# Optimization experiments

Hardware: AMD Instinct MI355X
Metric: run time of the kernel (lower is better)

Reference implementation:

```python
import jax, jax.numpy as jnp
import numpy as np

D_STATE = 16
DT_RANK = 4


def selective_scan(u, delta, A, Bc, Cc, D):
    """Mamba selective scan.
    u, delta: [S, L, d]; A: [d, N]; Bc, Cc: [S, L, N]; D: [d].
    Returns y: [S, L, d].
    """
    # discretize: deltaA [S,L,d,N], deltaB*u [S,L,d,N]
    dA = jnp.exp(delta[..., None] * A)
    dBu = (delta * u)[..., None] * Bc[:, :, None, :]

    def step(h, inp):
        dA_t, dBu_t, C_t = inp  # [S,d,N], [S,d,N], [S,N]
        h = dA_t * h + dBu_t
        y = jnp.einsum('sdn,sn->sd', h, C_t)
        return h, y

    S, L, d = u.shape
    N = A.shape[1]
    h0 = jnp.zeros((S, d, N), u.dtype)
    _, ys = jax.lax.scan(
        step, h0,
        (dA.transpose(1, 0, 2, 3), dBu.transpose(1, 0, 2, 3), Cc.transpose(1, 0, 2)))
    y = ys.transpose(1, 0, 2)  # [S, L, d]
    return y + u * D


def ssm_branch(u, A_log, D, x_proj_w, dt_proj_w, dt_proj_b):
    """u: [S, L, d] sequence of tokens; applies input-dependent SSM."""
    N = A_log.shape[1]
    proj = jnp.einsum('sld,pd->slp', u, x_proj_w)  # [S,L,dt_rank+2N]
    dt_raw = proj[..., :DT_RANK]
    Bc = proj[..., DT_RANK:DT_RANK + N]
    Cc = proj[..., DT_RANK + N:]
    delta = jax.nn.softplus(jnp.einsum('slr,dr->sld', dt_raw, dt_proj_w) + dt_proj_b)
    A = -jnp.exp(A_log)  # [d, N]
    return selective_scan(u, delta, A, Bc, Cc, D)


def setup_inputs() -> dict:
    key = jax.random.key(0)
    ks = jax.random.split(key, 6)
    B, C, H, W = 4, 64, 128, 128
    x = jax.random.normal(ks[0], (B, C, H, W), jnp.float32)
    A_log = jnp.log(jax.random.uniform(ks[1], (C, D_STATE), jnp.float32, 0.5, 4.0))
    D = jax.random.normal(ks[2], (C,), jnp.float32)
    x_proj_w = jax.random.normal(ks[3], (DT_RANK + 2 * D_STATE, C), jnp.float32) * (C ** -0.5)
    dt_proj_w = jax.random.normal(ks[4], (C, DT_RANK), jnp.float32) * (DT_RANK ** -0.5)
    dt_proj_b = jax.random.normal(ks[5], (C,), jnp.float32) * 0.1
    return {"x": x, "A_log": A_log, "D": D, "x_proj_w": x_proj_w,
            "dt_proj_w": dt_proj_w, "dt_proj_b": dt_proj_b}


def reference(x, A_log, D, x_proj_w, dt_proj_w, dt_proj_b):
    B, C, H, W = x.shape
    # horizontal scan: B*H row-sequences of length W
    u_h = x.transpose(0, 2, 3, 1).reshape(B * H, W, C)
    y_h = ssm_branch(u_h, A_log, D, x_proj_w, dt_proj_w, dt_proj_b)
    y_h = y_h.reshape(B, H, W, C).transpose(0, 3, 1, 2)
    # vertical scan: B*W column-sequences of length H
    u_v = x.transpose(0, 3, 2, 1).reshape(B * W, H, C)
    y_v = ssm_branch(u_v, A_log, D, x_proj_w, dt_proj_w, dt_proj_b)
    y_v = y_v.reshape(B, W, H, C).transpose(0, 3, 2, 1)
    return y_h + y_v
```

## Files before the change

kernel.cpp:

```cpp
#include <hip/hip_runtime.h>

#define BB 4
#define CC 64
#define HH 128
#define WW 128
#define NN 16
#define HW (HH*WW)

#if __has_builtin(__builtin_amdgcn_exp2f)
#define EXP2F(x) __builtin_amdgcn_exp2f(x)
#else
#define EXP2F(x) exp2f(x)
#endif

__device__ __forceinline__ float softplus_f(float x) {
    float e = __expf(-fabsf(x));
    return fmaxf(x, 0.0f) + __logf(1.0f + e);
}

__device__ __forceinline__ float2 f2mul(float2 a, float2 b) {
    return make_float2(a.x * b.x, a.y * b.y);
}
__device__ __forceinline__ float2 f2fma(float2 a, float2 b, float2 c) {
    return make_float2(fmaf(a.x, b.x, c.x), fmaf(a.y, b.y, c.y));
}

__global__ __launch_bounds__(256) void k_scan(
    const float* __restrict__ x, const float* __restrict__ xpw,
    const float* __restrict__ A_log, const float* __restrict__ Dv,
    const float* __restrict__ dtw, const float* __restrict__ dtb,
    float* __restrict__ out, float* __restrict__ yv)
{
    __shared__ float xt[128 * 64];
    __shared__ float bcs[128 * 32];
    __shared__ float dtr[128 * 4];
    __shared__ float dlt[8 * 64];

    const int t = threadIdx.x;
    const int half = blockIdx.x >> 9;
    const int r9 = blockIdx.x & 511;
    const int b = r9 >> 7;
    const int L = r9 & 127;

    if (half == 0) {
#pragma unroll
        for (int k = 0; k < 8; ++k) {
            int i = k * 256 + t;
            int c = i >> 5, jq = i & 31;
            float4 v = *(const float4*)&x[((size_t)(b * CC + c) * HH + L) * WW + jq * 4];
            int j0 = jq * 4;
            xt[(j0 + 0) * 64 + ((c + j0 + 0) & 63)] = v.x;
            xt[(j0 + 1) * 64 + ((c + j0 + 1) & 63)] = v.y;
            xt[(j0 + 2) * 64 + ((c + j0 + 2) & 63)] = v.z;
            xt[(j0 + 3) * 64 + ((c + j0 + 3) & 63)] = v.w;
        }
    } else {
#pragma unroll
        for (int p = 0; p < 32; ++p) {
            int c = t & 63, j = p * 4 + (t >> 6);
            xt[j * 64 + ((c + j) & 63)] =
                x[((size_t)(b * CC + c) * HH + j) * WW + L];
        }
    }
    __syncthreads();

    {
        const int wv = t >> 6, lane = t & 63;
        const int pg2 = __builtin_amdgcn_readfirstlane(wv & 1);
        const int pix = (wv >> 1) * 64 + lane;
        const int p0 = pg2 * 18;
        const int sw = pix & 7;
        float acc[18];
#pragma unroll
        for (int j = 0; j < 18; ++j) acc[j] = 0.f;
        for (int c4 = 0; c4 < 16; ++c4) {
            float xv0 = xt[pix * 64 + ((c4 * 4 + 0 + pix) & 63)];
            float xv1 = xt[pix * 64 + ((c4 * 4 + 1 + pix) & 63)];
            float xv2 = xt[pix * 64 + ((c4 * 4 + 2 + pix) & 63)];
            float xv3 = xt[pix * 64 + ((c4 * 4 + 3 + pix) & 63)];
#pragma unroll
            for (int j = 0; j < 18; ++j) {
                float4 wq = *(const float4*)&xpw[(p0 + j) * CC + c4 * 4];
                acc[j] = fmaf(wq.x, xv0, fmaf(wq.y, xv1,
                         fmaf(wq.z, xv2, fmaf(wq.w, xv3, acc[j]))));
            }
        }
        float* bp = &bcs[pix * 32];
        if (pg2 == 0) {
            *(float4*)&dtr[pix * 4] = make_float4(acc[0], acc[1], acc[2], acc[3]);
            *(float4*)&bp[((0 ^ sw) << 2)] = make_float4(acc[4], acc[5], acc[6], acc[7]);
            *(float4*)&bp[((1 ^ sw) << 2)] = make_float4(acc[8], acc[9], acc[10], acc[11]);
            *(float4*)&bp[((2 ^ sw) << 2)] = make_float4(acc[12], acc[13], acc[14], acc[15]);
            bp[((3 ^ sw) << 2) + 0] = acc[16];
            bp[((3 ^ sw) << 2) + 1] = acc[17];
        } else {
            bp[((3 ^ sw) << 2) + 2] = acc[0];
            bp[((3 ^ sw) << 2) + 3] = acc[1];
            *(float4*)&bp[((4 ^ sw) << 2)] = make_float4(acc[2], acc[3], acc[4], acc[5]);
            *(float4*)&bp[((5 ^ sw) << 2)] = make_float4(acc[6], acc[7], acc[8], acc[9]);
            *(float4*)&bp[((6 ^ sw) << 2)] = make_float4(acc[10], acc[11], acc[12], acc[13]);
            *(float4*)&bp[((7 ^ sw) << 2)] = make_float4(acc[14], acc[15], acc[16], acc[17]);
        }
    }

    const int d = t >> 2, ng = t & 3, n0 = ng * 4;
    const float L2E = 1.44269504088896340736f;
    float A0 = -__expf(A_log[d * NN + n0 + 0]) * L2E;
    float A1 = -__expf(A_log[d * NN + n0 + 1]) * L2E;
    float A2 = -__expf(A_log[d * NN + n0 + 2]) * L2E;
    float A3 = -__expf(A_log[d * NN + n0 + 3]) * L2E;
    const float Dd = Dv[d];
    float2 h01 = make_float2(0.f, 0.f), h23 = make_float2(0.f, 0.f);
    const int dd = t & 63, jb = t >> 6;
    const float4 wt4 = *(const float4*)&dtw[dd * 4];
    const float bdd = dtb[dd];
    float* drow = (half == 0 ? out : yv) + ((size_t)(b * CC + d) * 128 + L) * 128;

    for (int ch = 0; ch < 16; ++ch) {
        __syncthreads();
#pragma unroll
        for (int k = 0; k < 2; ++k) {
            int jl = jb * 2 + k;
            float4 dr = *(const float4*)&dtr[(ch * 8 + jl) * 4];
            float draw = fmaf(dr.x, wt4.x, fmaf(dr.y, wt4.y,
                         fmaf(dr.z, wt4.z, fmaf(dr.w, wt4.w, bdd))));
            dlt[jl * 64 + dd] = softplus_f(draw);
        }
        __syncthreads();
        float y0 = 0.f, y1 = 0.f;
#pragma unroll
        for (int jl = 0; jl < 8; ++jl) {
            const int j = ch * 8 + jl;
            float delta = dlt[jl * 64 + d];
            float u = xt[j * 64 + ((d + j) & 63)];
            const int s = j & 7;
            float4 Bv = *(const float4*)&bcs[j * 32 + ((ng ^ s) << 2)];
            float4 Cv = *(const float4*)&bcs[j * 32 + (((4 + ng) ^ s) << 2)];
            float du = delta * u;
            float2 e01 = make_float2(EXP2F(delta * A0), EXP2F(delta * A1));
            float2 e23 = make_float2(EXP2F(delta * A2), EXP2F(delta * A3));
            float2 du2 = make_float2(du, du);
            h01 = f2fma(e01, h01, f2mul(du2, make_float2(Bv.x, Bv.y)));
            h23 = f2fma(e23, h23, f2mul(du2, make_float2(Bv.z, Bv.w)));
            float2 yt = f2fma(h23, make_float2(Cv.z, Cv.w),
                              f2mul(h01, make_float2(Cv.x, Cv.y)));
            float y = yt.x + yt.y;
            y += __shfl_xor(y, 1);
            y += __shfl_xor(y, 2);
            y = fmaf(u, Dd, y);
            if (ng == (jl >> 1)) { if (jl & 1) y1 = y; else y0 = y; }
        }
        *(float2*)&drow[ch * 8 + ng * 2] = make_float2(y0, y1);
    }
}

__global__ __launch_bounds__(256) void k_add(const float* __restrict__ yv,
                                             float* __restrict__ out)
{
    __shared__ float td[32 * 33];
    int t = threadIdx.x;
    int bc_ = blockIdx.x >> 4;
    int tb = blockIdx.x & 15;
    int w0 = (tb & 3) * 32;
    int h0 = (tb >> 2) * 32;
    const float* src = yv + (size_t)bc_ * HW;
    float* dst = out + (size_t)bc_ * HW;
    int r = t >> 3, q = t & 7;
    float4 v = *(const float4*)&src[(w0 + r) * HH + h0 + q * 4];
    td[r * 33 + q * 4 + 0] = v.x;
    td[r * 33 + q * 4 + 1] = v.y;
    td[r * 33 + q * 4 + 2] = v.z;
    td[r * 33 + q * 4 + 3] = v.w;
    __syncthreads();
    float* op = &dst[(h0 + r) * WW + w0 + q * 4];
    float4 o = *(float4*)op;
    o.x += td[(q * 4 + 0) * 33 + r];
    o.y += td[(q * 4 + 1) * 33 + r];
    o.z += td[(q * 4 + 2) * 33 + r];
    o.w += td[(q * 4 + 3) * 33 + r];
    *(float4*)op = o;
}

extern "C" void kernel_launch(void* const* d_in, const int* in_sizes, int n_in,
                              void* d_out, int out_size, void* d_ws, size_t ws_size,
                              hipStream_t stream) {
    const float* x     = (const float*)d_in[0];
    const float* A_log = (const float*)d_in[1];
    const float* Dv    = (const float*)d_in[2];
    const float* xpw   = (const float*)d_in[3];
    const float* dtw   = (const float*)d_in[4];
    const float* dtb   = (const float*)d_in[5];
    float* out = (float*)d_out;
    float* yv  = (float*)d_ws;

    k_scan<<<1024, 256, 0, stream>>>(x, xpw, A_log, Dv, dtw, dtb, out, yv);
    k_add <<<BB * CC * 16, 256, 0, stream>>>(yv, out);
}
```

Baseline: 149.9 us.

## Fuse vertical-scan accumulation into scan via atomics, drop transpose-add kernel

Splits the single scan launch into two sequential launches (horizontal, then vertical). The vertical pass accumulates its results directly into the output with atomicAdd instead of writing a workspace buffer. This removes the separate transpose-and-add kernel and its extra read/write of a full-size intermediate. In exchange, the vertical pass issues strided scalar atomics (stride 128 floats), which coalesce poorly, and the two halves can no longer overlap within one grid.

```diff
diff --git a/kernel.cpp b/kernel.cpp
--- a/kernel.cpp
+++ b/kernel.cpp
@@ -29,7 +29,7 @@
     const float* __restrict__ x, const float* __restrict__ xpw,
     const float* __restrict__ A_log, const float* __restrict__ Dv,
     const float* __restrict__ dtw, const float* __restrict__ dtb,
-    float* __restrict__ out, float* __restrict__ yv)
+    float* __restrict__ out, int half)
 {
     __shared__ float xt[128 * 64];
     __shared__ float bcs[128 * 32];
@@ -37,10 +37,8 @@
     __shared__ float dlt[8 * 64];
 
     const int t = threadIdx.x;
-    const int half = blockIdx.x >> 9;
-    const int r9 = blockIdx.x & 511;
-    const int b = r9 >> 7;
-    const int L = r9 & 127;
+    const int b = blockIdx.x >> 7;
+    const int L = blockIdx.x & 127;
 
     if (half == 0) {
 #pragma unroll
@@ -114,7 +112,8 @@
     const int dd = t & 63, jb = t >> 6;
     const float4 wt4 = *(const float4*)&dtw[dd * 4];
     const float bdd = dtb[dd];
-    float* drow = (half == 0 ? out : yv) + ((size_t)(b * CC + d) * 128 + L) * 128;
+    float* drow = out + ((size_t)(b * CC + d) * 128 + L) * 128;
+    float* dcol = out + ((size_t)(b * CC + d) * 128) * 128 + L;
 
     for (int ch = 0; ch < 16; ++ch) {
         __syncthreads();
@@ -150,35 +149,14 @@
             y = fmaf(u, Dd, y);
             if (ng == (jl >> 1)) { if (jl & 1) y1 = y; else y0 = y; }
         }
-        *(float2*)&drow[ch * 8 + ng * 2] = make_float2(y0, y1);
+        if (half == 0) {
+            *(float2*)&drow[ch * 8 + ng * 2] = make_float2(y0, y1);
+        } else {
+            const int hp = ch * 8 + ng * 2;
+            atomicAdd(&dcol[(size_t)hp * 128], y0);
+            atomicAdd(&dcol[(size_t)(hp + 1) * 128], y1);
+        }
     }
-}
-
-__global__ __launch_bounds__(256) void k_add(const float* __restrict__ yv,
-                                             float* __restrict__ out)
-{
-    __shared__ float td[32 * 33];
-    int t = threadIdx.x;
-    int bc_ = blockIdx.x >> 4;
-    int tb = blockIdx.x & 15;
-    int w0 = (tb & 3) * 32;
-    int h0 = (tb >> 2) * 32;
-    const float* src = yv + (size_t)bc_ * HW;
-    float* dst = out + (size_t)bc_ * HW;
-    int r = t >> 3, q = t & 7;
-    float4 v = *(const float4*)&src[(w0 + r) * HH + h0 + q * 4];
-    td[r * 33 + q * 4 + 0] = v.x;
-    td[r * 33 + q * 4 + 1] = v.y;
-    td[r * 33 + q * 4 + 2] = v.z;
-    td[r * 33 + q * 4 + 3] = v.w;
-    __syncthreads();
-    float* op = &dst[(h0 + r) * WW + w0 + q * 4];
-    float4 o = *(float4*)op;
-    o.x += td[(q * 4 + 0) * 33 + r];
-    o.y += td[(q * 4 + 1) * 33 + r];
-    o.z += td[(q * 4 + 2) * 33 + r];
-    o.w += td[(q * 4 + 3) * 33 + r];
-    *(float4*)op = o;
 }
 
 extern "C" void kernel_launch(void* const* d_in, const int* in_sizes, int n_in,
@@ -191,8 +169,7 @@
     const float* dtw   = (const float*)d_in[4];
     const float* dtb   = (const float*)d_in[5];
     float* out = (float*)d_out;
-    float* yv  = (float*)d_ws;
 
-    k_scan<<<1024, 256, 0, stream>>>(x, xpw, A_log, Dv, dtw, dtb, out, yv);
-    k_add <<<BB * CC * 16, 256, 0, stream>>>(yv, out);
+    k_scan<<<512, 256, 0, stream>>>(x, xpw, A_log, Dv, dtw, dtb, out, 0);
+    k_scan<<<512, 256, 0, stream>>>(x, xpw, A_log, Dv, dtw, dtb, out, 1);
 }
```

New measurement: 333.3 us. 2.22x slower.

## Compute delta per quad in registers and broadcast via DPP, removing per-chunk barriers

Applied to the files above, without the earlier changes.

Each chunk previously had a cooperative step that computed delta into a shared array, with two __syncthreads around it. Now the four threads of each channel quad each compute the softplus delta for two timesteps in registers. The value is broadcast across the quad with DPP quad_perm moves, so the shared buffer and both per-chunk barriers go away. The chunk loop is also kept rolled, with a sched_barrier. This trades block-wide synchronisation and LDS traffic for some redundant delta computation across the 4x channel duplication.

```diff
diff --git a/kernel.cpp b/kernel.cpp
--- a/kernel.cpp
+++ b/kernel.cpp
@@ -23,6 +23,12 @@
 }
 __device__ __forceinline__ float2 f2fma(float2 a, float2 b, float2 c) {
     return make_float2(fmaf(a.x, b.x, c.x), fmaf(a.y, b.y, c.y));
+}
+
+template<int SRC>
+__device__ __forceinline__ float quad_bcast(float v) {
+    return __int_as_float(__builtin_amdgcn_mov_dpp(
+        __float_as_int(v), SRC * 0x55, 0xF, 0xF, true));
 }
 
 __global__ __launch_bounds__(256) void k_scan(
@@ -34,7 +40,6 @@
     __shared__ float xt[128 * 64];
     __shared__ float bcs[128 * 32];
     __shared__ float dtr[128 * 4];
-    __shared__ float dlt[8 * 64];
 
     const int t = threadIdx.x;
     const int half = blockIdx.x >> 9;
@@ -102,6 +107,7 @@
             *(float4*)&bp[((7 ^ sw) << 2)] = make_float4(acc[14], acc[15], acc[16], acc[17]);
         }
     }
+    __syncthreads();
 
     const int d = t >> 2, ng = t & 3, n0 = ng * 4;
     const float L2E = 1.44269504088896340736f;
@@ -111,47 +117,47 @@
     float A3 = -__expf(A_log[d * NN + n0 + 3]) * L2E;
     const float Dd = Dv[d];
     float2 h01 = make_float2(0.f, 0.f), h23 = make_float2(0.f, 0.f);
-    const int dd = t & 63, jb = t >> 6;
-    const float4 wt4 = *(const float4*)&dtw[dd * 4];
-    const float bdd = dtb[dd];
+    const float4 wt4d = *(const float4*)&dtw[d * 4];
+    const float bddd = dtb[d];
     float* drow = (half == 0 ? out : yv) + ((size_t)(b * CC + d) * 128 + L) * 128;
 
+#define SCAN_STEP(JL, DSRC)                                                    \
+    {                                                                          \
+        float delta = quad_bcast<(JL) & 3>(DSRC);                              \
+        const int jj = ch * 8 + (JL);                                          \
+        float u = xt[jj * 64 + ((d + jj) & 63)];                               \
+        float4 Bv = *(const float4*)&bcs[jj * 32 + ((ng ^ (JL)) << 2)];        \
+        float4 Cv = *(const float4*)&bcs[jj * 32 + (((4 + ng) ^ (JL)) << 2)];  \
+        float du = delta * u;                                                  \
+        float2 e01 = make_float2(EXP2F(delta * A0), EXP2F(delta * A1));        \
+        float2 e23 = make_float2(EXP2F(delta * A2), EXP2F(delta * A3));        \
+        float2 du2 = make_float2(du, du);                                      \
+        h01 = f2fma(e01, h01, f2mul(du2, make_float2(Bv.x, Bv.y)));            \
+        h23 = f2fma(e23, h23, f2mul(du2, make_float2(Bv.z, Bv.w)));            \
+        float2 yt = f2fma(h23, make_float2(Cv.z, Cv.w),                        \
+                          f2mul(h01, make_float2(Cv.x, Cv.y)));                \
+        float y = yt.x + yt.y;                                                 \
+        y += __shfl_xor(y, 1);                                                 \
+        y += __shfl_xor(y, 2);                                                 \
+        y = fmaf(u, Dd, y);                                                    \
+        if (ng == ((JL) >> 1)) { if ((JL) & 1) y1 = y; else y0 = y; }          \
+    }
+
+#pragma unroll 1
     for (int ch = 0; ch < 16; ++ch) {
-        __syncthreads();
-#pragma unroll
-        for (int k = 0; k < 2; ++k) {
-            int jl = jb * 2 + k;
-            float4 dr = *(const float4*)&dtr[(ch * 8 + jl) * 4];
-            float draw = fmaf(dr.x, wt4.x, fmaf(dr.y, wt4.y,
-                         fmaf(dr.z, wt4.z, fmaf(dr.w, wt4.w, bdd))));
-            dlt[jl * 64 + dd] = softplus_f(draw);
-        }
-        __syncthreads();
+        float4 drA = *(const float4*)&dtr[(ch * 8 + ng) * 4];
+        float4 drB = *(const float4*)&dtr[(ch * 8 + 4 + ng) * 4];
+        float da = softplus_f(fmaf(drA.x, wt4d.x, fmaf(drA.y, wt4d.y,
+                   fmaf(drA.z, wt4d.z, fmaf(drA.w, wt4d.w, bddd)))));
+        float db = softplus_f(fmaf(drB.x, wt4d.x, fmaf(drB.y, wt4d.y,
+                   fmaf(drB.z, wt4d.z, fmaf(drB.w, wt4d.w, bddd)))));
         float y0 = 0.f, y1 = 0.f;
-#pragma unroll
-        for (int jl = 0; jl < 8; ++jl) {
-            const int j = ch * 8 + jl;
-            float delta = dlt[jl * 64 + d];
-            float u = xt[j * 64 + ((d + j) & 63)];
-            const int s = j & 7;
-            float4 Bv = *(const float4*)&bcs[j * 32 + ((ng ^ s) << 2)];
-            float4 Cv = *(const float4*)&bcs[j * 32 + (((4 + ng) ^ s) << 2)];
-            float du = delta * u;
-            float2 e01 = make_float2(EXP2F(delta * A0), EXP2F(delta * A1));
-            float2 e23 = make_float2(EXP2F(delta * A2), EXP2F(delta * A3));
-            float2 du2 = make_float2(du, du);
-            h01 = f2fma(e01, h01, f2mul(du2, make_float2(Bv.x, Bv.y)));
-            h23 = f2fma(e23, h23, f2mul(du2, make_float2(Bv.z, Bv.w)));
-            float2 yt = f2fma(h23, make_float2(Cv.z, Cv.w),
-                              f2mul(h01, make_float2(Cv.x, Cv.y)));
-            float y = yt.x + yt.y;
-            y += __shfl_xor(y, 1);
-            y += __shfl_xor(y, 2);
-            y = fmaf(u, Dd, y);
-            if (ng == (jl >> 1)) { if (jl & 1) y1 = y; else y0 = y; }
-        }
+        SCAN_STEP(0, da) SCAN_STEP(1, da) SCAN_STEP(2, da) SCAN_STEP(3, da)
+        SCAN_STEP(4, db) SCAN_STEP(5, db) SCAN_STEP(6, db) SCAN_STEP(7, db)
         *(float2*)&drow[ch * 8 + ng * 2] = make_float2(y0, y1);
-    }
+        __builtin_amdgcn_sched_barrier(0);
+    }
+#undef SCAN_STEP
 }
 
 __global__ __launch_bounds__(256) void k_add(const float* __restrict__ yv,
```

Measured after the change: 144.0 us. -4.0%, faster.
